# Kernel optimization log

Measured on AMD Instinct MI355X. Metric: run time of the kernel, lower is better.

Reference implementation:

```python
import jax, jax.numpy as jnp
import numpy as np

D = 128      # n_hidden
NC = 4       # n_chan
DEPTH = 2
VD_DEPTH = 1
VD_ATTACH = 0
NV = 100000  # n_verts
PE_LEVELS = 6


def _mlp(x, Ws, bs):
    # MLP: Linear -> ReLU -> Linear -> ReLU -> Linear
    h = jax.nn.relu(x @ Ws[0] + bs[0])
    h = jax.nn.relu(h @ Ws[1] + bs[1])
    return h @ Ws[2] + bs[2]


def setup_inputs() -> dict:
    key = jax.random.key(0)
    ks = jax.random.split(key, 20)
    N, H, W = 2, 512, 512
    inp = {}
    inp["vert_idx_img"] = jax.random.randint(ks[0], (N, H, W, 3), 0, NV, dtype=jnp.int64) if jax.config.read("jax_enable_x64") else jax.random.randint(ks[0], (N, H, W, 3), 0, NV, dtype=jnp.int32)
    inp["bary_img"] = jax.random.uniform(ks[1], (N, H, W, 3), dtype=jnp.float32)
    inp["view_dir"] = jax.random.normal(ks[2], (N, H, W, 3), dtype=jnp.float32)
    # params
    s = D ** (-0.5)
    inp["emb_table"] = jax.random.normal(ks[3], (NV + 1, D), dtype=jnp.float32) * s
    k_lin = np.sqrt(2.0 / D).astype(np.float32)
    inp["vde_W"] = jax.random.normal(ks[4], (3 * PE_LEVELS, D), dtype=jnp.float32) * np.sqrt(2.0 / (3 * PE_LEVELS)).astype(np.float32)
    inp["vde_b"] = jnp.zeros((D,), jnp.float32)
    inp["vh_W"] = jax.random.normal(ks[5], (VD_DEPTH, 3, D, D), dtype=jnp.float32) * k_lin
    inp["vh_b"] = jnp.zeros((VD_DEPTH, 3, D), jnp.float32)
    inp["hid_W"] = jax.random.normal(ks[6], (DEPTH, 3, D, D), dtype=jnp.float32) * k_lin
    inp["hid_b"] = jnp.zeros((DEPTH, 3, D), jnp.float32)
    inp["head_W0"] = jax.random.normal(ks[7], (D, D), dtype=jnp.float32) * k_lin
    inp["head_b0"] = jnp.zeros((D,), jnp.float32)
    inp["head_W1"] = jax.random.normal(ks[8], (D, D), dtype=jnp.float32) * k_lin
    inp["head_b1"] = jnp.zeros((D,), jnp.float32)
    inp["head_W2"] = jax.random.normal(ks[9], (D, NC), dtype=jnp.float32) * k_lin
    inp["head_b2"] = jnp.zeros((NC,), jnp.float32)
    return inp


def reference(vert_idx_img, bary_img, view_dir, emb_table, vde_W, vde_b, vh_W, vh_b,
              hid_W, hid_b, head_W0, head_b0, head_W1, head_b1, head_W2, head_b2):
    # --- embedding gather with max_norm=1.0 renorm (torch nn.Embedding semantics)
    idx = vert_idx_img + 1                       # [N,H,W,3]
    e = emb_table[idx]                           # [N,H,W,3,D]
    nrm = jnp.linalg.norm(e, axis=-1, keepdims=True)
    e = e * jnp.where(nrm > 1.0, 1.0 / (nrm + 1e-7), 1.0)
    # --- barycentric weighted sum over the 3 face vertices
    v = jnp.sum(e * bary_img[..., None], axis=3)  # [N,H,W,D]
    # --- view-direction sin/cos positional encoding (proj_dims=6, val=0.9)
    ll = PE_LEVELS // 2
    exb = 2.0 * jnp.arange(ll, dtype=jnp.float32) / PE_LEVELS
    sigma = 2.0 * jnp.pi / jnp.power(0.9, exb)    # [3]
    pe = view_dir[..., None] * sigma              # [N,H,W,3,3]
    pe = jnp.concatenate([jnp.sin(pe), jnp.cos(pe)], axis=-1)  # [N,H,W,3,6]
    pe = pe.reshape(pe.shape[:-2] + (3 * PE_LEVELS,))           # [N,H,W,18]
    vh = pe @ vde_W + vde_b                       # [N,H,W,D]
    for i in range(vh_W.shape[0]):
        vh = jax.nn.relu(_mlp(vh, vh_W[i], vh_b[i]))
    # --- hidden MLP chain with view-dir modulation at viewdirs_attach
    h = v
    for i in range(hid_W.shape[0]):
        h = jax.nn.relu(_mlp(h, hid_W[i], hid_b[i]))
        if i == VD_ATTACH:
            h = h * vh
    # --- head MLP -> rgba
    rgb = _mlp(h, (head_W0, head_W1, head_W2), (head_b0, head_b1, head_b2))
    return rgb
```

## Files before the change

kernel.cpp:

```cpp
#include <hip/hip_runtime.h>

typedef unsigned int  u32;
typedef unsigned long long u64;
typedef unsigned short u16;
typedef __attribute__((ext_vector_type(8))) _Float16 h8;
typedef __attribute__((ext_vector_type(2))) _Float16 h2;
typedef __attribute__((ext_vector_type(4))) float    f4;

#define RS    136
#define PRS   40
#define PIXB  128
#define WOFF  5120
#define FULLT 16384
#define MFMA16 __builtin_amdgcn_mfma_f32_16x16x32_f16

__device__ __forceinline__ u16 f2h(float f) {
  _Float16 h = (_Float16)f;
  return __builtin_bit_cast(u16, h);
}
__device__ __forceinline__ u32 pkrtz(float a, float b) {
  return __builtin_bit_cast(u32, __builtin_amdgcn_cvt_pkrtz(a, b));
}
__device__ __forceinline__ u32 pkmul(u32 a, u32 b) {
  h2 r = __builtin_bit_cast(h2, a) * __builtin_bit_cast(h2, b);
  return __builtin_bit_cast(u32, r);
}
__device__ __forceinline__ u32 pkmax0(u32 a) {
  h2 z = {(_Float16)0.f, (_Float16)0.f};
  h2 r = __builtin_elementwise_max(__builtin_bit_cast(h2, a), z);
  return __builtin_bit_cast(u32, r);
}

__global__ __launch_bounds__(256) void rc_prep(
    const float* __restrict__ vde_W, const float* __restrict__ vh_W,
    const float* __restrict__ hid_W, const float* __restrict__ head_W0,
    const float* __restrict__ head_W1, const float* __restrict__ head_W2,
    u16* __restrict__ ws)
{
  const int TOT = WOFF + 12 * FULLT;
  int i = blockIdx.x * 256 + threadIdx.x;
  if (i >= TOT) return;
  float val = 0.f;
  if (i < WOFF) {
    int n = i / PRS, k = i - n * PRS;
    if (k < 18) val = vde_W[k * 128 + n];
  } else {
    int t  = i - WOFF;
    int j  = t >> 14;
    int c  = t & 16383;
    int nt = c >> 11;
    int ks = (c >> 9) & 3;
    int ln = (c >> 3) & 63;
    int e  = c & 7;
    int r  = ln & 15, g = ln >> 4;
    int n  = nt * 16 + r;
    int k  = ks * 32 + g * 8 + e;
    if (j < 3)        val = vh_W[j * 16384 + k * 128 + n];
    else if (j < 9)   val = hid_W[(j - 3) * 16384 + k * 128 + n];
    else if (j == 9)  val = head_W0[k * 128 + n];
    else if (j == 10) val = head_W1[k * 128 + n];
    else              val = (n < 4) ? head_W2[k * 4 + n] : 0.f;
  }
  ws[i] = f2h(val);
}

#define GLOAD(dst, base, voff, immstr)                                        \
  asm volatile("global_load_dwordx4 %0, %1, %2 offset:" immstr               \
               : "=v"(dst) : "v"(voff), "s"(base) : "memory")

#define ISSUE(S, NTL) do {                                                    \
  u32 vo_ = aoff + (NTL) * 4096;                                              \
  GLOAD(Ar##S[0], wbase, vo_, "0");                                           \
  GLOAD(Ar##S[1], wbase, vo_, "1024");                                        \
  GLOAD(Ar##S[2], wbase, vo_, "2048");                                        \
  GLOAD(Ar##S[3], wbase, vo_, "3072");                                        \
} while (0)

#define WAITV(nstr) do {                                                      \
  asm volatile("s_waitcnt vmcnt(" nstr ")" ::: "memory");                     \
  __builtin_amdgcn_sched_barrier(0);                                          \
} while (0)

#define EPI(NTL, AC, XNB) do {                                                \
  const int col = nbase + (NTL) * 16 + 4 * g;                                 \
  _Pragma("unroll")                                                           \
  for (int t = 0; t < 4; ++t) {                                               \
    u32 lo = pkmax0(pkrtz(AC[t][0], AC[t][1]));                               \
    u32 hi = pkmax0(pkrtz(AC[t][2], AC[t][3]));                               \
    if (mode == 1) {                                 \
      vhp[t][NTL][0] = lo; vhp[t][NTL][1] = hi;                               \
    } else {                                                                  \
      if (mode == 2) {                                \
        lo = pkmul(lo, vhp[t][NTL][0]);                                       \
        hi = pkmul(hi, vhp[t][NTL][1]);                                       \
      }                                                                       \
      *(uint2*)&XNB[xr[t] + col] = make_uint2(lo, hi);                        \
    }                                                                         \
  }                                                                           \
} while (0)

#define LAYER(LI, XC, XN) do {                                                \
  const int li   = (LI);                                                      \
  const int blb  = (li + 1) * 128;                                            \
  const int mode = (li == 2) ? 1 : (li == 5) ? 2 : 0;                         \
  const u64 wbase = (u64)(uintptr_t)(ws + WOFF + li * FULLT);                 \
  ISSUE(0, 0); ISSUE(1, 1);                            \
  f4 b0 = *(const f4*)&BL[blb + nbase + 4 * g];                               \
  f4 b1 = *(const f4*)&BL[blb + nbase + 16 + 4 * g];                          \
  f4 ac0[4] = {b0, b0, b0, b0};                                               \
  f4 ac1[4] = {b1, b1, b1, b1};                                               \
  _Pragma("unroll")                                                           \
  for (int ks = 0; ks < 4; ++ks) {                                            \
    h8 xk0 = *(const h8*)&XC[xr[0] + ks * 32 + g * 8];                        \
    h8 xk1 = *(const h8*)&XC[xr[1] + ks * 32 + g * 8];                        \
    h8 xk2 = *(const h8*)&XC[xr[2] + ks * 32 + g * 8];                        \
    h8 xk3 = *(const h8*)&XC[xr[3] + ks * 32 + g * 8];                        \
    if (ks == 0) WAITV("4");                                  \
    ac0[0] = MFMA16(Ar0[ks], xk0, ac0[0], 0, 0, 0);                           \
    ac0[1] = MFMA16(Ar0[ks], xk1, ac0[1], 0, 0, 0);                           \
    ac0[2] = MFMA16(Ar0[ks], xk2, ac0[2], 0, 0, 0);                           \
    ac0[3] = MFMA16(Ar0[ks], xk3, ac0[3], 0, 0, 0);                           \
    if (ks == 0) WAITV("0");           \
    ac1[0] = MFMA16(Ar1[ks], xk0, ac1[0], 0, 0, 0);                           \
    ac1[1] = MFMA16(Ar1[ks], xk1, ac1[1], 0, 0, 0);                           \
    ac1[2] = MFMA16(Ar1[ks], xk2, ac1[2], 0, 0, 0);                           \
    ac1[3] = MFMA16(Ar1[ks], xk3, ac1[3], 0, 0, 0);                           \
  }                                                                           \
  EPI(0, ac0, XN);                                                            \
  EPI(1, ac1, XN);                                                            \
  if (li == 2) do_gather(XN);                                                 \
  __syncthreads();                             \
} while (0)

__global__ __launch_bounds__(512, 4) void rc_main(
    const int*   __restrict__ vert,  const float* __restrict__ bary,
    const float* __restrict__ view,  const float* __restrict__ emb,
    const float* __restrict__ vde_b, const float* __restrict__ vh_b,
    const float* __restrict__ hid_b, const float* __restrict__ head_b0,
    const float* __restrict__ head_b1, const float* __restrict__ head_b2,
    const u16*   __restrict__ ws,    float* __restrict__ out)
{
  __shared__ __align__(16) u16   X0[PIXB * RS];
  __shared__ __align__(16) u16   X1[PIXB * RS];
  __shared__ __align__(16) float BL[1664];

  const int tid  = threadIdx.x;
  const int lane = tid & 63;
  const int w    = tid >> 6;
  const int pg   = w >> 2;
  const int cq   = w & 3;
  const int r    = lane & 15;
  const int g    = lane >> 4;
  const int pbase = pg * 64;
  const int nbase = cq * 32;
  const u32 aoff  = (u32)(cq * 8192 + lane * 16);
  const size_t bpix = (size_t)blockIdx.x * PIXB;

  for (int i = tid; i < 1664; i += 512) {
    float v;
    if      (i < 128)  v = vde_b[i];
    else if (i < 512)  v = vh_b[i - 128];
    else if (i < 1280) v = hid_b[i - 512];
    else if (i < 1408) v = head_b0[i - 1280];
    else if (i < 1536) v = head_b1[i - 1408];
    else if (i < 1540) v = head_b2[i - 1536];
    else               v = 0.f;
    BL[i] = v;
  }

  if (tid < PIXB) {
    const int p = tid;
    const float* vd = view + (bpix + p) * 3;
    const float SG0 = 6.28318530718f;
    const float SG1 = 6.50777324f;
    const float SG2 = 6.74038866f;
    u32 pw[16];
#pragma unroll
    for (int i = 0; i < 3; ++i) {
      float x = vd[i];
      float s0 = __sinf(x * SG0), c0 = __cosf(x * SG0);
      float s1 = __sinf(x * SG1), c1 = __cosf(x * SG1);
      float s2 = __sinf(x * SG2), c2 = __cosf(x * SG2);
      pw[i * 3 + 0] = (u32)f2h(s0) | ((u32)f2h(s1) << 16);
      pw[i * 3 + 1] = (u32)f2h(s2) | ((u32)f2h(c0) << 16);
      pw[i * 3 + 2] = (u32)f2h(c1) | ((u32)f2h(c2) << 16);
    }
#pragma unroll
    for (int q = 9; q < 16; ++q) pw[q] = 0u;
    uint4* dst = (uint4*)&X0[p * RS];
#pragma unroll
    for (int q = 0; q < 4; ++q)
      dst[q] = make_uint4(pw[4*q], pw[4*q+1], pw[4*q+2], pw[4*q+3]);
  }
  __syncthreads();

  const int xr[4] = { (pbase +      r) * RS, (pbase + 16 + r) * RS,
                      (pbase + 32 + r) * RS, (pbase + 48 + r) * RS };

  auto do_gather = [&](u16* XNB) {
#pragma unroll 4
    for (int i = 0; i < 4; ++i) {
      int p = w * 16 + g * 4 + i;
      size_t gp = bpix + p;
      const int*   vi = vert + gp * 3;
      const float* by = bary + gp * 3;
      f4 va = {0.f,0.f,0.f,0.f}, vb = {0.f,0.f,0.f,0.f};
#pragma unroll
      for (int vt = 0; vt < 3; ++vt) {
        int id = vi[vt] + 1;
        const float* row = emb + (size_t)id * 128 + r * 8;
        f4 e0 = *(const f4*)row;
        f4 e1 = *(const f4*)(row + 4);
        float ss = e0[0]*e0[0] + e0[1]*e0[1] + e0[2]*e0[2] + e0[3]*e0[3]
                 + e1[0]*e1[0] + e1[1]*e1[1] + e1[2]*e1[2] + e1[3]*e1[3];
        ss += __shfl_xor(ss, 1);
        ss += __shfl_xor(ss, 2);
        ss += __shfl_xor(ss, 4);
        ss += __shfl_xor(ss, 8);
        float nrm = sqrtf(ss);
        float sc  = (nrm > 1.f) ? (1.f / (nrm + 1e-7f)) : 1.f;
        float wt  = by[vt] * sc;
#pragma unroll
        for (int j = 0; j < 4; ++j) { va[j] += wt * e0[j]; vb[j] += wt * e1[j]; }
      }
      h8 o;
#pragma unroll
      for (int j = 0; j < 4; ++j) { o[j] = (_Float16)va[j]; o[j+4] = (_Float16)vb[j]; }
      *(h8*)&XNB[p * RS + r * 8] = o;
    }
  };

  {
    h8 Av[2];
#pragma unroll
    for (int ntl = 0; ntl < 2; ++ntl)
      Av[ntl] = *(const h8*)&ws[(nbase + ntl * 16 + r) * PRS + g * 8];
    h8 pe[4];
#pragma unroll
    for (int t = 0; t < 4; ++t) pe[t] = *(const h8*)&X0[xr[t] + g * 8];
#pragma unroll
    for (int ntl = 0; ntl < 2; ++ntl) {
      f4 bini = *(const f4*)&BL[nbase + ntl * 16 + 4 * g];
      const int col = nbase + ntl * 16 + 4 * g;
#pragma unroll
      for (int t = 0; t < 4; ++t) {
        f4 acc = MFMA16(Av[ntl], pe[t], bini, 0, 0, 0);
        *(uint2*)&X1[xr[t] + col] =
          make_uint2(pkrtz(acc[0], acc[1]), pkrtz(acc[2], acc[3]));
      }
    }
  }
  __syncthreads();

  u32 vhp[4][2][2];
  h8 Ar0[4], Ar1[4];
  LAYER(0, X1, X0);  LAYER(1, X0, X1);
  LAYER(2, X1, X0);  LAYER(3, X0, X1);
  LAYER(4, X1, X0);  LAYER(5, X0, X1);
  LAYER(6, X1, X0);  LAYER(7, X0, X1);
  LAYER(8, X1, X0);  LAYER(9, X0, X1);
  LAYER(10, X1, X0);

  if (cq == 0) {
    const u16* wa = ws + WOFF + 11 * FULLT;
    f4 b2 = *(const f4*)&BL[1536 + 4 * g];
    f4 acc[4] = {b2, b2, b2, b2};
#pragma unroll
    for (int ks = 0; ks < 4; ++ks) {
      h8 A = *(const h8*)&wa[ks * 512 + lane * 8];
#pragma unroll
      for (int t = 0; t < 4; ++t) {
        h8 xt = *(const h8*)&X0[xr[t] + ks * 32 + g * 8];
        acc[t] = MFMA16(A, xt, acc[t], 0, 0, 0);
      }
    }
    if (g == 0) {
#pragma unroll
      for (int t = 0; t < 4; ++t)
        *(f4*)&out[(bpix + pbase + t * 16 + r) * 4] = acc[t];
    }
  }
}

extern "C" void kernel_launch(void* const* d_in, const int* in_sizes, int n_in,
                              void* d_out, int out_size, void* d_ws, size_t ws_size,
                              hipStream_t stream) {
  const int*   vert    = (const int*)  d_in[0];
  const float* bary    = (const float*)d_in[1];
  const float* view    = (const float*)d_in[2];
  const float* emb     = (const float*)d_in[3];
  const float* vde_W   = (const float*)d_in[4];
  const float* vde_b   = (const float*)d_in[5];
  const float* vh_W    = (const float*)d_in[6];
  const float* vh_b    = (const float*)d_in[7];
  const float* hid_W   = (const float*)d_in[8];
  const float* hid_b   = (const float*)d_in[9];
  const float* head_W0 = (const float*)d_in[10];
  const float* head_b0 = (const float*)d_in[11];
  const float* head_W1 = (const float*)d_in[12];
  const float* head_b1 = (const float*)d_in[13];
  const float* head_W2 = (const float*)d_in[14];
  const float* head_b2 = (const float*)d_in[15];
  u16* wsp = (u16*)d_ws;

  rc_prep<<<788, 256, 0, stream>>>(vde_W, vh_W, hid_W, head_W0, head_W1, head_W2, wsp);
  rc_main<<<4096, 512, 0, stream>>>(vert, bary, view, emb, vde_b, vh_b, hid_b,
                                    head_b0, head_b1, head_b2, wsp, (float*)d_out);
}
```

Baseline: 284.9 us.

## Single-buffer activation LDS and raise occupancy hint to six

Merges the two ping-pong LDS activation buffers into one, so each layer reads its input into registers, synchronises, then overwrites the same buffer with its output. This roughly halves shared memory per block so more blocks can be resident per CU. The launch-bounds waves-per-EU hint also goes from 4 to 6 to match. The cost is an extra barrier per layer, and the tighter register budget may cause spills around the MFMA accumulators and prefetched weights.

```diff
diff --git a/kernel.cpp b/kernel.cpp
--- a/kernel.cpp
+++ b/kernel.cpp
@@ -81,7 +81,7 @@
   __builtin_amdgcn_sched_barrier(0);                                          \
 } while (0)
 
-#define EPI(NTL, AC, XNB) do {                                                \
+#define EPI(NTL, AC) do {                                                     \
   const int col = nbase + (NTL) * 16 + 4 * g;                                 \
   _Pragma("unroll")                                                           \
   for (int t = 0; t < 4; ++t) {                                               \
@@ -94,12 +94,12 @@
         lo = pkmul(lo, vhp[t][NTL][0]);                                       \
         hi = pkmul(hi, vhp[t][NTL][1]);                                       \
       }                                                                       \
-      *(uint2*)&XNB[xr[t] + col] = make_uint2(lo, hi);                        \
+      *(uint2*)&X[xr[t] + col] = make_uint2(lo, hi);                          \
     }                                                                         \
   }                                                                           \
 } while (0)
 
-#define LAYER(LI, XC, XN) do {                                                \
+#define LAYER(LI) do {                                                        \
   const int li   = (LI);                                                      \
   const int blb  = (li + 1) * 128;                                            \
   const int mode = (li == 2) ? 1 : (li == 5) ? 2 : 0;                         \
@@ -111,10 +111,10 @@
   f4 ac1[4] = {b1, b1, b1, b1};                                               \
   _Pragma("unroll")                                                           \
   for (int ks = 0; ks < 4; ++ks) {                                            \
-    h8 xk0 = *(const h8*)&XC[xr[0] + ks * 32 + g * 8];                        \
-    h8 xk1 = *(const h8*)&XC[xr[1] + ks * 32 + g * 8];                        \
-    h8 xk2 = *(const h8*)&XC[xr[2] + ks * 32 + g * 8];                        \
-    h8 xk3 = *(const h8*)&XC[xr[3] + ks * 32 + g * 8];                        \
+    h8 xk0 = *(const h8*)&X[xr[0] + ks * 32 + g * 8];                         \
+    h8 xk1 = *(const h8*)&X[xr[1] + ks * 32 + g * 8];                         \
+    h8 xk2 = *(const h8*)&X[xr[2] + ks * 32 + g * 8];                         \
+    h8 xk3 = *(const h8*)&X[xr[3] + ks * 32 + g * 8];                         \
     if (ks == 0) WAITV("4");                                  \
     ac0[0] = MFMA16(Ar0[ks], xk0, ac0[0], 0, 0, 0);                           \
     ac0[1] = MFMA16(Ar0[ks], xk1, ac0[1], 0, 0, 0);                           \
@@ -126,13 +126,14 @@
     ac1[2] = MFMA16(Ar1[ks], xk2, ac1[2], 0, 0, 0);                           \
     ac1[3] = MFMA16(Ar1[ks], xk3, ac1[3], 0, 0, 0);                           \
   }                                                                           \
-  EPI(0, ac0, XN);                                                            \
-  EPI(1, ac1, XN);                                                            \
-  if (li == 2) do_gather(XN);                                                 \
-  __syncthreads();                             \
+  __syncthreads();                           \
+  EPI(0, ac0);                                                                \
+  EPI(1, ac1);                                                                \
+  if (li == 2) do_gather();                                                   \
+  __syncthreads();                                    \
 } while (0)
 
-__global__ __launch_bounds__(512, 4) void rc_main(
+__global__ __launch_bounds__(512, 6) void rc_main(
     const int*   __restrict__ vert,  const float* __restrict__ bary,
     const float* __restrict__ view,  const float* __restrict__ emb,
     const float* __restrict__ vde_b, const float* __restrict__ vh_b,
@@ -140,8 +141,7 @@
     const float* __restrict__ head_b1, const float* __restrict__ head_b2,
     const u16*   __restrict__ ws,    float* __restrict__ out)
 {
-  __shared__ __align__(16) u16   X0[PIXB * RS];
-  __shared__ __align__(16) u16   X1[PIXB * RS];
+  __shared__ __align__(16) u16   X[PIXB * RS];
   __shared__ __align__(16) float BL[1664];
 
   const int tid  = threadIdx.x;
@@ -187,7 +187,7 @@
     }
 #pragma unroll
     for (int q = 9; q < 16; ++q) pw[q] = 0u;
-    uint4* dst = (uint4*)&X0[p * RS];
+    uint4* dst = (uint4*)&X[p * RS];
 #pragma unroll
     for (int q = 0; q < 4; ++q)
       dst[q] = make_uint4(pw[4*q], pw[4*q+1], pw[4*q+2], pw[4*q+3]);
@@ -197,7 +197,7 @@
   const int xr[4] = { (pbase +      r) * RS, (pbase + 16 + r) * RS,
                       (pbase + 32 + r) * RS, (pbase + 48 + r) * RS };
 
-  auto do_gather = [&](u16* XNB) {
+  auto do_gather = [&]() {
 #pragma unroll 4
     for (int i = 0; i < 4; ++i) {
       int p = w * 16 + g * 4 + i;
@@ -226,7 +226,7 @@
       h8 o;
 #pragma unroll
       for (int j = 0; j < 4; ++j) { o[j] = (_Float16)va[j]; o[j+4] = (_Float16)vb[j]; }
-      *(h8*)&XNB[p * RS + r * 8] = o;
+      *(h8*)&X[p * RS + r * 8] = o;
     }
   };
 
@@ -237,7 +237,8 @@
       Av[ntl] = *(const h8*)&ws[(nbase + ntl * 16 + r) * PRS + g * 8];
     h8 pe[4];
 #pragma unroll
-    for (int t = 0; t < 4; ++t) pe[t] = *(const h8*)&X0[xr[t] + g * 8];
+    for (int t = 0; t < 4; ++t) pe[t] = *(const h8*)&X[xr[t] + g * 8];
+    __syncthreads();
 #pragma unroll
     for (int ntl = 0; ntl < 2; ++ntl) {
       f4 bini = *(const f4*)&BL[nbase + ntl * 16 + 4 * g];
@@ -245,7 +246,7 @@
 #pragma unroll
       for (int t = 0; t < 4; ++t) {
         f4 acc = MFMA16(Av[ntl], pe[t], bini, 0, 0, 0);
-        *(uint2*)&X1[xr[t] + col] =
+        *(uint2*)&X[xr[t] + col] =
           make_uint2(pkrtz(acc[0], acc[1]), pkrtz(acc[2], acc[3]));
       }
     }
@@ -254,12 +255,9 @@
 
   u32 vhp[4][2][2];
   h8 Ar0[4], Ar1[4];
-  LAYER(0, X1, X0);  LAYER(1, X0, X1);
-  LAYER(2, X1, X0);  LAYER(3, X0, X1);
-  LAYER(4, X1, X0);  LAYER(5, X0, X1);
-  LAYER(6, X1, X0);  LAYER(7, X0, X1);
-  LAYER(8, X1, X0);  LAYER(9, X0, X1);
-  LAYER(10, X1, X0);
+  LAYER(0);  LAYER(1);  LAYER(2);  LAYER(3);
+  LAYER(4);  LAYER(5);  LAYER(6);  LAYER(7);
+  LAYER(8);  LAYER(9);  LAYER(10);
 
   if (cq == 0) {
     const u16* wa = ws + WOFF + 11 * FULLT;
@@ -270,7 +268,7 @@
       h8 A = *(const h8*)&wa[ks * 512 + lane * 8];
 #pragma unroll
       for (int t = 0; t < 4; ++t) {
-        h8 xt = *(const h8*)&X0[xr[t] + ks * 32 + g * 8];
+        h8 xt = *(const h8*)&X[xr[t] + ks * 32 + g * 8];
         acc[t] = MFMA16(A, xt, acc[t], 0, 0, 0);
       }
     }
```

Result: slower. 326.6 us (+14.7%).
